# Performance work log

Measured on AMD Instinct MI355X. Metric: run time of the kernel, lower is better.

Reference implementation:

```python
import jax, jax.numpy as jnp
import numpy as np

B, N, C, H, R = 16, 1024, 768, 12, 16
HD = C // H
SCALE = HD ** -0.5


def setup_inputs() -> dict:
    key = jax.random.key(0)
    ks = jax.random.split(key, 13)
    f = lambda k, shape, s=0.02: jax.random.normal(k, shape, dtype=jnp.float32) * s
    return {
        "x": jax.random.normal(ks[0], (B, N, C), dtype=jnp.float32),
        "W_qkv": f(ks[1], (3 * C, C)),
        "b_qkv": f(ks[2], (3 * C,)),
        "W_proj": f(ks[3], (C, C)),
        "b_proj": f(ks[4], (C,)),
        "A_q": f(ks[5], (R, C)),
        "B_q": f(ks[6], (C, R)),
        "A_k": f(ks[7], (R, C)),
        "B_k": f(ks[8], (C, R)),
        "A_v": f(ks[9], (R, C)),
        "B_v": f(ks[10], (C, R)),
        "A_o": f(ks[11], (R, C)),
        "B_o": f(ks[12], (C, R)),
    }


def _lora(x, A, Bu):
    # Adapter with no norm/act/bias, scaling=1.0: low-rank x @ A^T @ B^T
    return (x @ A.T) @ Bu.T


def _heads(t):
    # [B, N, C] -> [B, H, N, HD]
    return t.reshape(B, N, H, HD).transpose(0, 2, 1, 3)


def reference(x, W_qkv, b_qkv, W_proj, b_proj, A_q, B_q, A_k, B_k, A_v, B_v, A_o, B_o):
    qkv = x @ W_qkv.T + b_qkv                    # [B, N, 3C]
    qkv = qkv.reshape(B, N, 3, H, HD).transpose(2, 0, 3, 1, 4)  # [3, B, H, N, HD]
    q, k, v = qkv[0], qkv[1], qkv[2]
    q = q + _heads(_lora(x, A_q, B_q))
    k = k + _heads(_lora(x, A_k, B_k))
    v = v + _heads(_lora(x, A_v, B_v))
    attn = jnp.einsum("bhnd,bhmd->bhnm", q, k) * SCALE
    attn = jax.nn.softmax(attn, axis=-1)
    out = jnp.einsum("bhnm,bhmd->bhnd", attn, v)  # [B, H, N, HD]
    out = out.transpose(0, 2, 1, 3).reshape(B, N, C)
    out = out @ W_proj.T + b_proj
    out = out + _lora(out, A_o, B_o)
    return out
```

## Files before the change

### kernel.cpp

```cpp
#include <hip/hip_runtime.h>
#include <cmath>


#define DEVI __device__ __forceinline__

typedef float f32x4 __attribute__((ext_vector_type(4)));
typedef float f32x16 __attribute__((ext_vector_type(16)));
typedef short s16x8 __attribute__((ext_vector_type(8)));
typedef __bf16 b16x8 __attribute__((ext_vector_type(8)));
typedef unsigned int u32x4 __attribute__((ext_vector_type(4)));

static constexpr int MTOT = 16384;
static constexpr int C = 768;
static constexpr int N3 = 2304;

DEVI unsigned short f2bf(float x) {
  unsigned int u = __builtin_bit_cast(unsigned int, x);
  return (unsigned short)((u + 0x7FFFu + ((u >> 16) & 1u)) >> 16);
}

DEVI f32x16 mfma32(s16x8 a, s16x8 b, f32x16 c) {
  return __builtin_amdgcn_mfma_f32_32x32x16_bf16(
      __builtin_bit_cast(b16x8, a), __builtin_bit_cast(b16x8, b), c, 0, 0, 0);
}

DEVI void async16(const void* g, void* l) {
  __builtin_amdgcn_global_load_lds(
      (__attribute__((address_space(1))) void*)g,
      (__attribute__((address_space(3))) void*)l, 16, 0, 0);
}

DEVI unsigned cvtpk_bf16(float lo, float hi2) {
  unsigned r;
  asm("v_cvt_pk_bf16_f32 %0, %1, %2" : "=v"(r) : "v"(lo), "v"(hi2));
  return r;
}


__global__ __launch_bounds__(256) void k_prep_x(const float* __restrict__ x,
                                                unsigned short* __restrict__ xb) {
  int idx = (blockIdx.x * 256 + threadIdx.x) * 4;
  float4 v = *(const float4*)(x + idx);
  uint2 p;
  p.x = (unsigned int)f2bf(v.x) | ((unsigned int)f2bf(v.y) << 16);
  p.y = (unsigned int)f2bf(v.z) | ((unsigned int)f2bf(v.w) << 16);
  *(uint2*)(xb + idx) = p;
}

__global__ __launch_bounds__(256) void k_prep_wqkv(
    const float* __restrict__ W, const float* __restrict__ Aq,
    const float* __restrict__ Bq, const float* __restrict__ Ak,
    const float* __restrict__ Bk, const float* __restrict__ Av,
    const float* __restrict__ Bv, unsigned short* __restrict__ out) {
  int idx = blockIdx.x * 256 + threadIdx.x;
  int n = idx / 768, c = idx - n * 768;
  int s = n / 768, co = n - s * 768;
  const float* A = (s == 0) ? Aq : (s == 1) ? Ak : Av;
  const float* Bm = (s == 0) ? Bq : (s == 1) ? Bk : Bv;
  float acc = W[idx];
#pragma unroll
  for (int r = 0; r < 16; ++r) acc += Bm[co * 16 + r] * A[r * 768 + c];
  out[idx] = f2bf(acc);
}

__global__ __launch_bounds__(256) void k_prep_M(const float* __restrict__ Ao,
                                                const float* __restrict__ Wp,
                                                float* __restrict__ M) {
  __shared__ float red[4][64];
  const int r = blockIdx.x, j0 = blockIdx.y * 64;
  const int jl = threadIdx.x & 63, cs = threadIdx.x >> 6;
  float acc = 0.f;
#pragma unroll 4
  for (int c = cs * 192; c < cs * 192 + 192; ++c)
    acc += Ao[r * 768 + c] * Wp[c * 768 + j0 + jl];
  red[cs][jl] = acc;
  __syncthreads();
  if (cs == 0)
    M[r * 768 + j0 + jl] = red[0][jl] + red[1][jl] + red[2][jl] + red[3][jl];
}

__global__ __launch_bounds__(256) void k_prep_wpe(const float* __restrict__ Wp,
                                                  const float* __restrict__ Bo,
                                                  const float* __restrict__ M,
                                                  unsigned short* __restrict__ out) {
  int idx = blockIdx.x * 256 + threadIdx.x;
  int n = idx / 768, j = idx - n * 768;
  float acc = Wp[idx];
#pragma unroll
  for (int r = 0; r < 16; ++r) acc += Bo[n * 16 + r] * M[r * 768 + j];
  out[idx] = f2bf(acc);
}

__global__ __launch_bounds__(256) void k_prep_beff(const float* __restrict__ bp,
                                                   const float* __restrict__ Ao,
                                                   const float* __restrict__ Bo,
                                                   float* __restrict__ beff) {
  __shared__ float red[256];
  __shared__ float bv[16];
  const int t = threadIdx.x;
  const int r = t >> 4, cs = t & 15;
  float a = 0.f;
#pragma unroll 4
  for (int c = cs * 48; c < cs * 48 + 48; ++c) a += Ao[r * 768 + c] * bp[c];
  red[t] = a;
  __syncthreads();
  if (cs == 0) {
    float s = 0.f;
#pragma unroll
    for (int k = 0; k < 16; ++k) s += red[r * 16 + k];
    bv[r] = s;
  }
  __syncthreads();
#pragma unroll
  for (int it = 0; it < 3; ++it) {
    const int n = it * 256 + t;
    float acc = bp[n];
#pragma unroll
    for (int r2 = 0; r2 < 16; ++r2) acc += Bo[n * 16 + r2] * bv[r2];
    beff[n] = acc;
  }
}


template <bool SWAP>
DEVI void g256_core(const unsigned short* __restrict__ Ag,
                    const unsigned short* __restrict__ Bg,
                    short* lds, f32x16 (&acc)[4][2]) {
  const int t = threadIdx.x;
  const int w = t >> 6, l = t & 63;
  const int wm = w >> 2, wn = w & 3, lc = l & 31, hi = l >> 5;

  int aoff[4][4], boff[2][4];
#pragma unroll
  for (int mi = 0; mi < 4; ++mi)
#pragma unroll
    for (int kc = 0; kc < 4; ++kc) {
      const int rr = mi * 32 + lc;
      aoff[mi][kc] = wm * 8192 + rr * 64 + (((kc * 2 + hi) ^ (rr & 7)) * 8);
    }
#pragma unroll
  for (int nd = 0; nd < 2; ++nd)
#pragma unroll
    for (int kc = 0; kc < 4; ++kc) {
      const int rr = (wn & 1) * 64 + nd * 32 + lc;
      boff[nd][kc] =
          16384 + (wn >> 1) * 8192 + rr * 64 + (((kc * 2 + hi) ^ (rr & 7)) * 8);
    }

  auto stageHT = [&](const unsigned short* G, int row0, int k0, int lbase) {
#pragma unroll
    for (int it = 0; it < 2; ++it) {
      const int s16 = it * 512 + t;
      const int rr = s16 >> 3;
      const int cg = (s16 & 7) ^ (rr & 7);
      async16(G + (size_t)(row0 + rr) * 768 + k0 + cg * 8, lds + lbase + s16 * 8);
    }
  };

  stageHT(Ag, 0, 0, 0);
  stageHT(Ag, 128, 0, 8192);
  stageHT(Bg, 0, 0, 16384);
  stageHT(Bg, 128, 0, 24576);
  stageHT(Bg, 0, 64, 32768 + 16384);
  stageHT(Bg, 128, 64, 32768 + 24576);
  asm volatile("s_waitcnt vmcnt(4)" ::: "memory");
  asm volatile("s_barrier" ::: "memory");

  for (int i = 0; i < 6; ++i) {
    const int kY1 = (2 * i + 1) * 64;
    const int kX2 = (2 * i + 2) * 64;
    const int kY3 = (2 * i + 3) * 64;
    const bool stX = (2 * i + 2) <= 11;
    const bool stY = (2 * i + 3) <= 11;
    s16x8 bf[2][4];
#pragma unroll
    for (int ph = 0; ph < 8; ++ph) {
      const int tp = ph & 3;
      const int cb = (ph < 4) ? 0 : 32768;
      if (tp == 0) {
#pragma unroll
        for (int nd = 0; nd < 2; ++nd)
#pragma unroll
          for (int kc = 0; kc < 4; ++kc)
            bf[nd][kc] = *(const s16x8*)&lds[cb + boff[nd][kc]];
      }
      s16x8 af[4];
#pragma unroll
      for (int kc = 0; kc < 4; ++kc)
        af[kc] = *(const s16x8*)&lds[cb + aoff[tp][kc]];
      if (ph == 0) stageHT(Ag, 0, kY1, 32768);
      if (ph == 1) stageHT(Ag, 128, kY1, 32768 + 8192);
      if (ph == 2 && stX) stageHT(Bg, 0, kX2, 16384);
      if (ph == 3 && stX) stageHT(Bg, 128, kX2, 24576);
      if (ph == 4 && stX) stageHT(Ag, 0, kX2, 0);
      if (ph == 5 && stX) stageHT(Ag, 128, kX2, 8192);
      if (ph == 6 && stY) stageHT(Bg, 0, kY3, 32768 + 16384);
      if (ph == 7 && stY) stageHT(Bg, 128, kY3, 32768 + 24576);
      asm volatile("s_barrier" ::: "memory");
      __builtin_amdgcn_s_setprio(1);
#pragma unroll
      for (int kc = 0; kc < 4; ++kc)
#pragma unroll
        for (int nd = 0; nd < 2; ++nd) {
          if constexpr (SWAP)
            acc[tp][nd] = mfma32(bf[nd][kc], af[kc], acc[tp][nd]);
          else
            acc[tp][nd] = mfma32(af[kc], bf[nd][kc], acc[tp][nd]);
        }
      __builtin_amdgcn_s_setprio(0);
      if (ph == 3) {
        if (stX)
          asm volatile("s_waitcnt vmcnt(4)" ::: "memory");
        else
          asm volatile("s_waitcnt vmcnt(0)" ::: "memory");
      }
      if (ph == 7)
        asm volatile("s_waitcnt vmcnt(4)" ::: "memory");
      asm volatile("s_barrier" ::: "memory");
    }
  }
}


__global__ __launch_bounds__(512, 2) void k_gemm_qkv256(
    const unsigned short* __restrict__ A, const unsigned short* __restrict__ Bw,
    const float* __restrict__ bias, unsigned short* __restrict__ qb,
    unsigned short* __restrict__ kb, unsigned short* __restrict__ vtb) {
  __shared__ short lds[65536];
  const int t = threadIdx.x;
  const int w = t >> 6, l = t & 63;
  const int wm = w >> 2, wn = w & 3, lc = l & 31, hi = l >> 5;
  const int mblk = blockIdx.x, nblk = blockIdx.y;
  const unsigned short* Ag = A + (size_t)(mblk * 256) * 768;
  const unsigned short* Bg = Bw + (size_t)(nblk * 256) * 768;
  f32x16 acc[4][2] = {};
  const int seg = nblk / 3;
  const float c1 = 0.18033688011112042f;

  if (seg < 2) {
    g256_core<true>(Ag, Bg, lds, acc);
    unsigned short* dst = (seg == 0) ? qb : kb;
    const float scl = (seg == 0) ? c1 : 1.0f;
#pragma unroll
    for (int nd = 0; nd < 2; ++nd)
#pragma unroll
      for (int q2 = 0; q2 < 4; ++q2) {
        const int n0 = nblk * 256 + wn * 64 + nd * 32 + q2 * 8 + 4 * hi;
        const int nrel = n0 - seg * 768;
        const int hh = nrel >> 6, d0 = nrel & 63;
        const float4 bv4 = *(const float4*)(bias + n0);
#pragma unroll
        for (int mi = 0; mi < 4; ++mi) {
          const int m = mblk * 256 + wm * 128 + mi * 32 + lc;
          const int b = m >> 10, pos = m & 1023;
          uint2 pk;
          pk.x = (unsigned int)f2bf((acc[mi][nd][4 * q2 + 0] + bv4.x) * scl) |
                 ((unsigned int)f2bf((acc[mi][nd][4 * q2 + 1] + bv4.y) * scl) << 16);
          pk.y = (unsigned int)f2bf((acc[mi][nd][4 * q2 + 2] + bv4.z) * scl) |
                 ((unsigned int)f2bf((acc[mi][nd][4 * q2 + 3] + bv4.w) * scl) << 16);
          *(uint2*)&dst[(size_t)((b * 12 + hh) * 1024 + pos) * 64 + d0] = pk;
        }
      }
  } else {
    g256_core<false>(Ag, Bg, lds, acc);
#pragma unroll
    for (int nd = 0; nd < 2; ++nd) {
      const int n = nblk * 256 + wn * 64 + nd * 32 + lc;
      const int nrel = n - 1536;
      const int hh = nrel >> 6, d = nrel & 63;
      const float bvv = bias[n];
#pragma unroll
      for (int mi = 0; mi < 4; ++mi)
#pragma unroll
        for (int q2 = 0; q2 < 4; ++q2) {
          const int m0 = mblk * 256 + wm * 128 + mi * 32 + q2 * 8 + 4 * hi;
          const int b = m0 >> 10, pos0 = m0 & 1023;
          uint2 pk;
          pk.x = (unsigned int)f2bf(acc[mi][nd][4 * q2 + 0] + bvv) |
                 ((unsigned int)f2bf(acc[mi][nd][4 * q2 + 1] + bvv) << 16);
          pk.y = (unsigned int)f2bf(acc[mi][nd][4 * q2 + 2] + bvv) |
                 ((unsigned int)f2bf(acc[mi][nd][4 * q2 + 3] + bvv) << 16);
          *(uint2*)&vtb[(size_t)((b * 12 + hh) * 64 + d) * 1024 + pos0] = pk;
        }
    }
  }
}


__global__ __launch_bounds__(512, 2) void k_gemm_proj256(
    const unsigned short* __restrict__ A, const unsigned short* __restrict__ Bw,
    const float* __restrict__ bias, float* __restrict__ out) {
  __shared__ short lds[65536];
  const int t = threadIdx.x;
  const int w = t >> 6, l = t & 63;
  const int wm = w >> 2, wn = w & 3, lc = l & 31, hi = l >> 5;
  const int mblk = blockIdx.x, nblk = blockIdx.y;
  const unsigned short* Ag = A + (size_t)(mblk * 256) * 768;
  const unsigned short* Bg = Bw + (size_t)(nblk * 256) * 768;
  f32x16 acc[4][2] = {};
  g256_core<true>(Ag, Bg, lds, acc);
#pragma unroll
  for (int nd = 0; nd < 2; ++nd)
#pragma unroll
    for (int q2 = 0; q2 < 4; ++q2) {
      const int n0 = nblk * 256 + wn * 64 + nd * 32 + q2 * 8 + 4 * hi;
      const float4 bv4 = *(const float4*)(bias + n0);
#pragma unroll
      for (int mi = 0; mi < 4; ++mi) {
        const int m = mblk * 256 + wm * 128 + mi * 32 + lc;
        float4 o;
        o.x = acc[mi][nd][4 * q2 + 0] + bv4.x;
        o.y = acc[mi][nd][4 * q2 + 1] + bv4.y;
        o.z = acc[mi][nd][4 * q2 + 2] + bv4.z;
        o.w = acc[mi][nd][4 * q2 + 3] + bv4.w;
        *(float4*)&out[(size_t)m * 768 + n0] = o;
      }
    }
}


__global__ __launch_bounds__(256, 2) void k_attn(
    const unsigned short* __restrict__ qg, const unsigned short* __restrict__ kg,
    const unsigned short* __restrict__ vtg, unsigned short* __restrict__ og) {
  __shared__ short k_lds[2][64 * 64];
  __shared__ short vt_lds[2][64 * 64];

  const int t = threadIdx.x;
  const int w = t >> 6, l = t & 63;
  const int lc = l & 31;
  const int hi = l >> 5;
  const int bh = blockIdx.x;
  const int qpair = blockIdx.y;
  const int h = bh % 12, b = bh / 12;

  const unsigned short* Qg = qg + (size_t)(bh * 1024 + qpair * 256) * 64;
  const unsigned short* Kg = kg + (size_t)bh * 1024 * 64;
  const unsigned short* Vtg = vtg + (size_t)bh * 64 * 1024;

  const int srl = l >> 3;
  const int sgc = (l & 7) ^ srl;

  s16x8 qfA[4], qfB[4];
#pragma unroll
  for (int kc = 0; kc < 4; ++kc) {
    qfA[kc] = *(const s16x8*)(Qg + (w * 32 + lc) * 64 + kc * 16 + hi * 8);
    qfB[kc] = *(const s16x8*)(Qg + (128 + w * 32 + lc) * 64 + kc * 16 + hi * 8);
  }

  int koffs[2][4];
#pragma unroll
  for (int pg = 0; pg < 2; ++pg)
#pragma unroll
    for (int kc = 0; kc < 4; ++kc)
      koffs[pg][kc] = (pg * 32 + lc) * 64 + (((kc * 2 + hi) ^ (lc & 7)) * 8);
  int voffs[2][4][2];
#pragma unroll
  for (int nd = 0; nd < 2; ++nd)
#pragma unroll
    for (int mi = 0; mi < 4; ++mi)
#pragma unroll
      for (int h2 = 0; h2 < 2; ++h2)
        voffs[nd][mi][h2] =
            (nd * 32 + lc) * 64 + (((2 * mi + h2) ^ (lc & 7)) * 8) + 4 * hi;

  auto stage = [&](int bufn, int tkv) {
#pragma unroll
    for (int it = 0; it < 2; ++it) {
      const int rbase = it * 32 + w * 8;
      async16(Kg + (size_t)(tkv * 64 + rbase + srl) * 64 + sgc * 8,
              &k_lds[bufn][rbase * 64]);
      async16(Vtg + (size_t)(rbase + srl) * 1024 + tkv * 64 + sgc * 8,
              &vt_lds[bufn][rbase * 64]);
    }
  };

  stage(0, 0);

  f32x16 oaccA[2] = {}, oaccB[2] = {};
  float llA = 0.f, llB = 0.f;

  for (int tkv = 0; tkv < 16; ++tkv) {
    const int buf = tkv & 1;
    __syncthreads();
    if (tkv < 15) stage(buf ^ 1, tkv + 1);

#pragma unroll
    for (int pg = 0; pg < 2; ++pg) {
      s16x8 ka[4];
#pragma unroll
      for (int kc = 0; kc < 4; ++kc)
        ka[kc] = *(const s16x8*)&k_lds[buf][koffs[pg][kc]];
      f32x16 stA = {}, stB = {};
#pragma unroll
      for (int kc = 0; kc < 4; ++kc) {
        stA = mfma32(ka[kc], qfA[kc], stA);
        stB = mfma32(ka[kc], qfB[kc], stB);
      }
      unsigned pkA[4][2], pkB[4][2];
#pragma unroll
      for (int q = 0; q < 4; ++q) {
        const float a0 = __builtin_amdgcn_exp2f(stA[4 * q + 0]);
        const float a1 = __builtin_amdgcn_exp2f(stA[4 * q + 1]);
        const float a2 = __builtin_amdgcn_exp2f(stA[4 * q + 2]);
        const float a3 = __builtin_amdgcn_exp2f(stA[4 * q + 3]);
        pkA[q][0] = cvtpk_bf16(a0, a1);
        pkA[q][1] = cvtpk_bf16(a2, a3);
        llA += (a0 + a1) + (a2 + a3);
        const float b0 = __builtin_amdgcn_exp2f(stB[4 * q + 0]);
        const float b1 = __builtin_amdgcn_exp2f(stB[4 * q + 1]);
        const float b2 = __builtin_amdgcn_exp2f(stB[4 * q + 2]);
        const float b3 = __builtin_amdgcn_exp2f(stB[4 * q + 3]);
        pkB[q][0] = cvtpk_bf16(b0, b1);
        pkB[q][1] = cvtpk_bf16(b2, b3);
        llB += (b0 + b1) + (b2 + b3);
      }
      __builtin_amdgcn_s_setprio(1);
#pragma unroll
      for (int m = 0; m < 2; ++m) {
        const int mi = pg * 2 + m;
        u32x4 faA, faB;
        faA[0] = pkA[2 * m][0];
        faA[1] = pkA[2 * m][1];
        faA[2] = pkA[2 * m + 1][0];
        faA[3] = pkA[2 * m + 1][1];
        faB[0] = pkB[2 * m][0];
        faB[1] = pkB[2 * m][1];
        faB[2] = pkB[2 * m + 1][0];
        faB[3] = pkB[2 * m + 1][1];
        const s16x8 pafA = __builtin_bit_cast(s16x8, faA);
        const s16x8 pafB = __builtin_bit_cast(s16x8, faB);
#pragma unroll
        for (int nd = 0; nd < 2; ++nd) {
          const uint2 vlo = *(const uint2*)&vt_lds[buf][voffs[nd][mi][0]];
          const uint2 vhi = *(const uint2*)&vt_lds[buf][voffs[nd][mi][1]];
          u32x4 vbu;
          vbu[0] = vlo.x;
          vbu[1] = vlo.y;
          vbu[2] = vhi.x;
          vbu[3] = vhi.y;
          const s16x8 vb = __builtin_bit_cast(s16x8, vbu);
          oaccA[nd] = mfma32(pafA, vb, oaccA[nd]);
          oaccB[nd] = mfma32(pafB, vb, oaccB[nd]);
        }
      }
      __builtin_amdgcn_s_setprio(0);
    }
  }

  const float lqA = llA + __shfl_xor(llA, 32, 64);
  const float lqB = llB + __shfl_xor(llB, 32, 64);
  float linvA[16], linvB[16];
#pragma unroll
  for (int r = 0; r < 16; ++r) {
    const int qr = (r & 3) + 8 * (r >> 2) + 4 * hi;
    linvA[r] = 1.0f / __shfl(lqA, qr, 64);
    linvB[r] = 1.0f / __shfl(lqB, qr, 64);
  }

  const int orow0 = qpair * 256 + w * 32;
#pragma unroll
  for (int nd = 0; nd < 2; ++nd)
#pragma unroll
    for (int r = 0; r < 16; ++r) {
      const int qr = (r & 3) + 8 * (r >> 2) + 4 * hi;
      const int d = nd * 32 + lc;
      og[(size_t)(b * 1024 + orow0 + qr) * 768 + h * 64 + d] =
          f2bf(oaccA[nd][r] * linvA[r]);
      og[(size_t)(b * 1024 + orow0 + 128 + qr) * 768 + h * 64 + d] =
          f2bf(oaccB[nd][r] * linvB[r]);
    }
}


extern "C" void kernel_launch(void* const* d_in, const int* in_sizes, int n_in,
                              void* d_out, int out_size, void* d_ws, size_t ws_size,
                              hipStream_t stream) {
  const float* x = (const float*)d_in[0];
  const float* Wqkv = (const float*)d_in[1];
  const float* bqkv = (const float*)d_in[2];
  const float* Wp = (const float*)d_in[3];
  const float* bp = (const float*)d_in[4];
  const float* Aq = (const float*)d_in[5];
  const float* Bq = (const float*)d_in[6];
  const float* Ak = (const float*)d_in[7];
  const float* Bk = (const float*)d_in[8];
  const float* Av = (const float*)d_in[9];
  const float* Bv = (const float*)d_in[10];
  const float* Ao = (const float*)d_in[11];
  const float* Bo = (const float*)d_in[12];
  float* out = (float*)d_out;

  unsigned short* xb = (unsigned short*)d_ws;
  unsigned short* wqkvb = xb + (size_t)MTOT * C;
  unsigned short* wpeb = wqkvb + (size_t)N3 * C;
  unsigned short* qb = wpeb + (size_t)C * C;
  unsigned short* kb = qb + (size_t)MTOT * C;
  unsigned short* vtb = kb + (size_t)MTOT * C;
  float* Mbuf = (float*)(vtb + (size_t)MTOT * C);
  float* beff = Mbuf + 16 * 768;
  unsigned short* ob = xb;

  k_prep_x<<<12288, 256, 0, stream>>>(x, xb);
  k_prep_wqkv<<<6912, 256, 0, stream>>>(Wqkv, Aq, Bq, Ak, Bk, Av, Bv, wqkvb);
  k_prep_M<<<dim3(16, 12), 256, 0, stream>>>(Ao, Wp, Mbuf);
  k_prep_wpe<<<2304, 256, 0, stream>>>(Wp, Bo, Mbuf, wpeb);
  k_prep_beff<<<1, 256, 0, stream>>>(bp, Ao, Bo, beff);

  k_gemm_qkv256<<<dim3(64, 9), 512, 0, stream>>>(xb, wqkvb, bqkv, qb, kb, vtb);
  k_attn<<<dim3(192, 4), 256, 0, stream>>>(qb, kb, vtb, ob);
  k_gemm_proj256<<<dim3(64, 3), 512, 0, stream>>>(ob, wpeb, beff, out);
}
```

Measured before the change: 364.0 us.

## Restructure 256x256 GEMM core into simple double-buffered k-tile pipeline

Replaces the 8-phase ping-pong schedule, which used split LDS buffers and staggered staging, with a plain double-buffered loop over 12 k-tiles. Each iteration loads all A and B fragments into registers, waits, stages tile kt+2 into the freed buffer, then runs all MFMAs. This cuts the barrier count per k-tile and simplifies address layout. The cost is higher register pressure from holding 16 A fragments, and the loop no longer interleaves LDS reads with MFMAs.

```diff
diff --git a/kernel.cpp b/kernel.cpp
--- a/kernel.cpp
+++ b/kernel.cpp
@@ -135,16 +135,15 @@
   for (int mi = 0; mi < 4; ++mi)
 #pragma unroll
     for (int kc = 0; kc < 4; ++kc) {
-      const int rr = mi * 32 + lc;
-      aoff[mi][kc] = wm * 8192 + rr * 64 + (((kc * 2 + hi) ^ (rr & 7)) * 8);
+      const int rr = wm * 128 + mi * 32 + lc;
+      aoff[mi][kc] = rr * 64 + (((kc * 2 + hi) ^ (rr & 7)) * 8);
     }
 #pragma unroll
   for (int nd = 0; nd < 2; ++nd)
 #pragma unroll
     for (int kc = 0; kc < 4; ++kc) {
-      const int rr = (wn & 1) * 64 + nd * 32 + lc;
-      boff[nd][kc] =
-          16384 + (wn >> 1) * 8192 + rr * 64 + (((kc * 2 + hi) ^ (rr & 7)) * 8);
+      const int rr = wn * 64 + nd * 32 + lc;
+      boff[nd][kc] = 16384 + rr * 64 + (((kc * 2 + hi) ^ (rr & 7)) * 8);
     }
 
   auto stageHT = [&](const unsigned short* G, int row0, int k0, int lbase) {
@@ -156,67 +155,55 @@
       async16(G + (size_t)(row0 + rr) * 768 + k0 + cg * 8, lds + lbase + s16 * 8);
     }
   };
-
-  stageHT(Ag, 0, 0, 0);
-  stageHT(Ag, 128, 0, 8192);
-  stageHT(Bg, 0, 0, 16384);
-  stageHT(Bg, 128, 0, 24576);
-  stageHT(Bg, 0, 64, 32768 + 16384);
-  stageHT(Bg, 128, 64, 32768 + 24576);
-  asm volatile("s_waitcnt vmcnt(4)" ::: "memory");
-  asm volatile("s_barrier" ::: "memory");
-
-  for (int i = 0; i < 6; ++i) {
-    const int kY1 = (2 * i + 1) * 64;
-    const int kX2 = (2 * i + 2) * 64;
-    const int kY3 = (2 * i + 3) * 64;
-    const bool stX = (2 * i + 2) <= 11;
-    const bool stY = (2 * i + 3) <= 11;
-    s16x8 bf[2][4];
-#pragma unroll
-    for (int ph = 0; ph < 8; ++ph) {
-      const int tp = ph & 3;
-      const int cb = (ph < 4) ? 0 : 32768;
-      if (tp == 0) {
-#pragma unroll
-        for (int nd = 0; nd < 2; ++nd)
-#pragma unroll
-          for (int kc = 0; kc < 4; ++kc)
-            bf[nd][kc] = *(const s16x8*)&lds[cb + boff[nd][kc]];
-      }
-      s16x8 af[4];
+  auto stageKT = [&](int kt, int base) {
+    const int k0 = kt * 64;
+    stageHT(Ag, 0, k0, base);
+    stageHT(Ag, 128, k0, base + 8192);
+    stageHT(Bg, 0, k0, base + 16384);
+    stageHT(Bg, 128, k0, base + 24576);
+  };
+
+  stageKT(0, 0);
+  stageKT(1, 32768);
+  asm volatile("s_waitcnt vmcnt(8)");
+  __builtin_amdgcn_s_barrier();
+
+  for (int kt = 0; kt < 12; ++kt) {
+    const int cb = (kt & 1) ? 32768 : 0;
+    s16x8 af[4][4], bf[2][4];
+#pragma unroll
+    for (int mi = 0; mi < 4; ++mi)
 #pragma unroll
       for (int kc = 0; kc < 4; ++kc)
-        af[kc] = *(const s16x8*)&lds[cb + aoff[tp][kc]];
-      if (ph == 0) stageHT(Ag, 0, kY1, 32768);
-      if (ph == 1) stageHT(Ag, 128, kY1, 32768 + 8192);
-      if (ph == 2 && stX) stageHT(Bg, 0, kX2, 16384);
-      if (ph == 3 && stX) stageHT(Bg, 128, kX2, 24576);
-      if (ph == 4 && stX) stageHT(Ag, 0, kX2, 0);
-      if (ph == 5 && stX) stageHT(Ag, 128, kX2, 8192);
-      if (ph == 6 && stY) stageHT(Bg, 0, kY3, 32768 + 16384);
-      if (ph == 7 && stY) stageHT(Bg, 128, kY3, 32768 + 24576);
-      asm volatile("s_barrier" ::: "memory");
-      __builtin_amdgcn_s_setprio(1);
+        af[mi][kc] = *(const s16x8*)&lds[cb + aoff[mi][kc]];
+#pragma unroll
+    for (int nd = 0; nd < 2; ++nd)
 #pragma unroll
       for (int kc = 0; kc < 4; ++kc)
+        bf[nd][kc] = *(const s16x8*)&lds[cb + boff[nd][kc]];
+    asm volatile("s_waitcnt lgkmcnt(0)");
+    __builtin_amdgcn_sched_barrier(0);
+    __builtin_amdgcn_s_barrier();
+    if (kt + 2 < 12) stageKT(kt + 2, cb);
+    __builtin_amdgcn_s_setprio(1);
+#pragma unroll
+    for (int kc = 0; kc < 4; ++kc)
+#pragma unroll
+      for (int mi = 0; mi < 4; ++mi)
 #pragma unroll
         for (int nd = 0; nd < 2; ++nd) {
           if constexpr (SWAP)
-            acc[tp][nd] = mfma32(bf[nd][kc], af[kc], acc[tp][nd]);
+            acc[mi][nd] = mfma32(bf[nd][kc], af[mi][kc], acc[mi][nd]);
           else
-            acc[tp][nd] = mfma32(af[kc], bf[nd][kc], acc[tp][nd]);
+            acc[mi][nd] = mfma32(af[mi][kc], bf[nd][kc], acc[mi][nd]);
         }
-      __builtin_amdgcn_s_setprio(0);
-      if (ph == 3) {
-        if (stX)
-          asm volatile("s_waitcnt vmcnt(4)" ::: "memory");
-        else
-          asm volatile("s_waitcnt vmcnt(0)" ::: "memory");
-      }
-      if (ph == 7)
-        asm volatile("s_waitcnt vmcnt(4)" ::: "memory");
-      asm volatile("s_barrier" ::: "memory");
+    __builtin_amdgcn_s_setprio(0);
+    if (kt < 11) {
+      if (kt + 2 < 12)
+        asm volatile("s_waitcnt vmcnt(8)");
+      else
+        asm volatile("s_waitcnt vmcnt(0)");
+      __builtin_amdgcn_s_barrier();
     }
   }
 }
```

Result: slower. 408.2 us (+12.1%).
